# Optimization experiments

Measured on AMD Instinct MI355X. Metric: run time of the kernel, lower is better.

The kernel has to match this reference:

```python
import jax, jax.numpy as jnp
import numpy as np

DIM = 1024
NUM_HEADS = 16
HEAD_DIM = DIM // NUM_HEADS
SCALE = HEAD_DIM ** -0.5
HIDDEN = int(DIM * 1.0)


def setup_inputs() -> dict:
    key = jax.random.key(0)
    ks = jax.random.split(key, 11)
    s = 0.02
    return {
        "x":  jax.random.normal(ks[0], (2, 2048, DIM), jnp.float32),
        "Wq": jax.random.normal(ks[1], (DIM, DIM), jnp.float32) * s,
        "bq": jnp.zeros((DIM,), jnp.float32),
        "Wk": jax.random.normal(ks[2], (DIM, DIM), jnp.float32) * s,
        "bk": jnp.zeros((DIM,), jnp.float32),
        "Wv": jax.random.normal(ks[3], (DIM, DIM), jnp.float32) * s,
        "bv": jnp.zeros((DIM,), jnp.float32),
        "W1": jax.random.normal(ks[4], (HIDDEN, DIM), jnp.float32) * s,
        "b1": jnp.zeros((HIDDEN,), jnp.float32),
        "W2": jax.random.normal(ks[5], (DIM, HIDDEN), jnp.float32) * s,
        "b2": jnp.zeros((DIM,), jnp.float32),
    }


def _split_heads(t, B, S):
    # [B,S,C] -> [B,H,S,hd]
    return t.reshape(B, S, NUM_HEADS, HEAD_DIM).transpose(0, 2, 1, 3)


def reference(x, Wq, bq, Wk, bk, Wv, bv, W1, b1, W2, b2):
    B, S, C = x.shape
    q = _split_heads(x @ Wq.T + bq, B, S) * SCALE
    k = _split_heads(x @ Wk.T + bk, B, S)
    v = _split_heads(x @ Wv.T + bv, B, S)
    # softmax-free bilinear attention, scores in float32 (matches .float())
    attn = jnp.einsum('bhqd,bhkd->bhqk', q.astype(jnp.float32), k.astype(jnp.float32))
    out = jnp.einsum('bhqk,bhkd->bhqd', attn, v)  # [B,H,S,hd]
    out = out.transpose(0, 2, 1, 3).reshape(B, S, C)
    h = jax.nn.gelu(out @ W1.T + b1, approximate=False)
    mlp = h @ W2.T + b2
    return x + out + mlp
```

## Files before the change

### kernel.cpp

```cpp
#include <hip/hip_runtime.h>
#include <math.h>

#define DIM    1024
#define BATCH  2
#define SEQ    2048
#define NHEAD  16
#define HDIM   64
#define MROWS  (BATCH*SEQ)
#define NSPLIT 8

typedef unsigned short u16;
typedef __attribute__((ext_vector_type(8))) short  s16x8;
typedef __attribute__((ext_vector_type(4))) float  f32x4;

__device__ __forceinline__ float bf2f(u16 h) {
    unsigned u = ((unsigned)h) << 16; float f; __builtin_memcpy(&f, &u, 4); return f;
}
__device__ __forceinline__ u16 f2bf(float f) {
    unsigned u; __builtin_memcpy(&u, &f, 4);
    u += 0x7FFFu + ((u >> 16) & 1u);
    return (u16)(u >> 16);
}

__device__ __forceinline__ void glds16(const u16* g, u16* l) {
    __builtin_amdgcn_global_load_lds(
        (const __attribute__((address_space(1))) void*)g,
        (__attribute__((address_space(3))) void*)l, 16, 0, 0);
}

__global__ __launch_bounds__(256)
void pack_all(const float* __restrict__ x,
              const float* __restrict__ Wq, const float* __restrict__ Wk,
              const float* __restrict__ Wv, const float* __restrict__ W1,
              const float* __restrict__ W2,
              u16* __restrict__ xb, u16* __restrict__ Wqb, u16* __restrict__ Wkb,
              u16* __restrict__ Wvb, u16* __restrict__ W1b, u16* __restrict__ W2b)
{
    const int bid = blockIdx.x;
    const float* src; u16* dst; int i;
    if (bid < 4096) { src = x; dst = xb; i = bid * 256 + threadIdx.x; }
    else {
        const int w = (bid - 4096) >> 10;
        const int lb = (bid - 4096) & 1023;
        src = (w == 0) ? Wq : (w == 1) ? Wk : (w == 2) ? Wv : (w == 3) ? W1 : W2;
        dst = (w == 0) ? Wqb : (w == 1) ? Wkb : (w == 2) ? Wvb : (w == 3) ? W1b : W2b;
        i = lb * 256 + threadIdx.x;
    }
    float4 v = ((const float4*)src)[i];
    ushort4 o = { f2bf(v.x), f2bf(v.y), f2bf(v.z), f2bf(v.w) };
    ((ushort4*)dst)[i] = o;
}

__device__ __forceinline__ void gemm_core_pf128(const u16* __restrict__ Ab,
                                                const u16* __restrict__ Bb,
                                                u16* As, u16* Bs,
                                                int tid, f32x4 acc[4][4])
{
    const int w = tid >> 6, l = tid & 63;
    const int wm = (w >> 1) * 64, wn = (w & 1) * 64;
    const int lr = l & 15, kq = l >> 4;

    const int srow = w * 16 + (l >> 2);
    const int scol = (l & 3) * 8;
    const u16* gA = Ab + (size_t)srow * DIM + scol;
    const u16* gB = Bb + (size_t)srow * DIM + scol;
    const int sdst = w * 512;

    glds16(gA, As + sdst);  glds16(gA + 64 * DIM, As + 2048 + sdst);
    glds16(gB, Bs + sdst);  glds16(gB + 64 * DIM, Bs + 2048 + sdst);

    const int NIT = DIM / 32;
    for (int it = 0; it < NIT; ++it) {
        __syncthreads();
        if (it + 1 < NIT) {
            const int k = (it + 1) * 32;
            u16* An = As + ((it + 1) & 1) * 4096 + sdst;
            u16* Bn = Bs + ((it + 1) & 1) * 4096 + sdst;
            glds16(gA + k, An);  glds16(gA + k + 64 * DIM, An + 2048);
            glds16(gB + k, Bn);  glds16(gB + k + 64 * DIM, Bn + 2048);
        }
        const u16* Ac = As + (it & 1) * 4096;
        const u16* Bc = Bs + (it & 1) * 4096;
        s16x8 af[4], bfr[4];
        #pragma unroll
        for (int i = 0; i < 4; ++i)
            af[i]  = *(const s16x8*)(Ac + (wm + i * 16 + lr) * 32 + kq * 8);
        #pragma unroll
        for (int j = 0; j < 4; ++j)
            bfr[j] = *(const s16x8*)(Bc + (wn + j * 16 + lr) * 32 + kq * 8);
        #pragma unroll
        for (int i = 0; i < 4; ++i)
            #pragma unroll
            for (int j = 0; j < 4; ++j)
                acc[i][j] = __builtin_amdgcn_mfma_f32_16x16x32_bf16(af[i], bfr[j], acc[i][j], 0, 0, 0);
    }
}

__device__ __forceinline__ void gemm_core_pf64(const u16* __restrict__ Ab,
                                               const u16* __restrict__ Bb,
                                               u16* As , u16* Bs ,
                                               int tid, f32x4 acc[2][4])
{
    const int w  = tid >> 6, l = tid & 63;
    const int wm = (w >> 1) * 32, wn = (w & 1) * 64;
    const int lr = l & 15, kq = l >> 4;

    const int srow = w * 16 + (l >> 2);
    const int scol = (l & 3) * 8;
    const u16* gA = Ab + (size_t)srow * DIM + scol;
    const u16* gB = Bb + (size_t)srow * DIM + scol;
    const int sdst = w * 512;

    glds16(gA, As + sdst);
    glds16(gB, Bs + sdst);  glds16(gB + 64 * DIM, Bs + 2048 + sdst);

    const int NIT = DIM / 32;
    for (int it = 0; it < NIT; ++it) {
        __syncthreads();
        if (it + 1 < NIT) {
            const int k = (it + 1) * 32;
            u16* An = As + ((it + 1) & 1) * 2048 + sdst;
            u16* Bn = Bs + ((it + 1) & 1) * 4096 + sdst;
            glds16(gA + k, An);
            glds16(gB + k, Bn);  glds16(gB + k + 64 * DIM, Bn + 2048);
        }
        const u16* Ac = As + (it & 1) * 2048;
        const u16* Bc = Bs + (it & 1) * 4096;
        s16x8 af[2], bfr[4];
        #pragma unroll
        for (int i = 0; i < 2; ++i)
            af[i]  = *(const s16x8*)(Ac + (wm + i * 16 + lr) * 32 + kq * 8);
        #pragma unroll
        for (int j = 0; j < 4; ++j)
            bfr[j] = *(const s16x8*)(Bc + (wn + j * 16 + lr) * 32 + kq * 8);
        #pragma unroll
        for (int i = 0; i < 2; ++i)
            #pragma unroll
            for (int j = 0; j < 4; ++j)
                acc[i][j] = __builtin_amdgcn_mfma_f32_16x16x32_bf16(af[i], bfr[j], acc[i][j], 0, 0, 0);
    }
}

__global__ __launch_bounds__(256)
void qkv_gemm(const u16* __restrict__ xb,
              const u16* __restrict__ Wq, const u16* __restrict__ Wk, const u16* __restrict__ Wv,
              const float* __restrict__ bq, const float* __restrict__ bk, const float* __restrict__ bv,
              u16* __restrict__ qo, u16* __restrict__ ko, u16* __restrict__ vo)
{
    __shared__ __align__(16) u16 SH[16384];
    const int tid = threadIdx.x;
    const int m0  = blockIdx.x * 128;
    const int sel = blockIdx.y >> 3;
    const int n0  = (blockIdx.y & 7) * 128;
    const u16*   B    = (sel == 0) ? Wq : (sel == 1) ? Wk : Wv;
    const float* bias = (sel == 0) ? bq : (sel == 1) ? bk : bv;
    u16*         C    = (sel == 0) ? qo : (sel == 1) ? ko : vo;
    const float scale = (sel == 0) ? 0.125f : 1.0f;

    f32x4 acc[4][4];
    #pragma unroll
    for (int i = 0; i < 4; ++i)
        #pragma unroll
        for (int j = 0; j < 4; ++j) acc[i][j] = (f32x4){0.f, 0.f, 0.f, 0.f};

    gemm_core_pf128(xb + (size_t)m0 * DIM, B + (size_t)n0 * DIM, SH, SH + 8192, tid, acc);

    __syncthreads();
    const int w = tid >> 6, l = tid & 63;
    const int wm = (w >> 1) * 64, wn = (w & 1) * 64;
    const int er = l >> 4, ec = l & 15;
    #pragma unroll
    for (int j = 0; j < 4; ++j) {
        const int colv = wn + j * 16 + ec;
        const float bb = bias[n0 + colv];
        const int cg = colv >> 3, cl = colv & 7;
        #pragma unroll
        for (int i = 0; i < 4; ++i)
            #pragma unroll
            for (int r = 0; r < 4; ++r) {
                const int row = wm + i * 16 + er * 4 + r;
                const int g = ((row >> 2) & 3) << 1;
                SH[row * 128 + ((cg ^ g) << 3) + cl] = f2bf((acc[i][j][r] + bb) * scale);
            }
    }
    __syncthreads();
    {
        const int cg = tid & 15, rr = tid >> 4;
        #pragma unroll
        for (int pass = 0; pass < 8; ++pass) {
            const int row = rr + (pass << 4);
            const int g = ((row >> 2) & 3) << 1;
            uint4 v = *(const uint4*)(SH + row * 128 + ((cg ^ g) << 3));
            *(uint4*)(C + (size_t)(m0 + row) * DIM + n0 + (cg << 3)) = v;
        }
    }
}

__global__ __launch_bounds__(256)
void gemm_bf16(const u16* __restrict__ A, const u16* __restrict__ B,
               const float* __restrict__ bias,
               u16* __restrict__ Cb, float* __restrict__ Cf,
               const float* __restrict__ rx, const u16* __restrict__ rattn,
               int mode)
{
    __shared__ __align__(16) u16 SH[12288];
    const int tid = threadIdx.x;
    const int m0 = blockIdx.x * 64, n0 = blockIdx.y * 128;

    f32x4 acc[2][4];
    #pragma unroll
    for (int i = 0; i < 2; ++i)
        #pragma unroll
        for (int j = 0; j < 4; ++j) acc[i][j] = (f32x4){0.f, 0.f, 0.f, 0.f};

    gemm_core_pf64(A + (size_t)m0 * DIM, B + (size_t)n0 * DIM, SH, SH + 4096, tid, acc);

    const int w = tid >> 6, l = tid & 63;
    const int wm = (w >> 1) * 32, wn = (w & 1) * 64;
    const int er = l >> 4, ec = l & 15;

    if (mode == 1) {
        __syncthreads();
        #pragma unroll
        for (int j = 0; j < 4; ++j) {
            const int colv = wn + j * 16 + ec;
            const float bb = bias[n0 + colv];
            const int cg = colv >> 3, cl = colv & 7;
            #pragma unroll
            for (int i = 0; i < 2; ++i)
                #pragma unroll
                for (int r = 0; r < 4; ++r) {
                    const int row = wm + i * 16 + er * 4 + r;
                    const int g = ((row >> 2) & 3) << 1;
                    float v = acc[i][j][r] + bb;
                    v = 0.5f * v * (1.0f + erff(v * 0.70710678118654752f));
                    SH[row * 128 + ((cg ^ g) << 3) + cl] = f2bf(v);
                }
        }
        __syncthreads();
        const int cg = tid & 15, rr = tid >> 4;
        #pragma unroll
        for (int pass = 0; pass < 4; ++pass) {
            const int row = rr + (pass << 4);
            const int g = ((row >> 2) & 3) << 1;
            uint4 v = *(const uint4*)(SH + row * 128 + ((cg ^ g) << 3));
            *(uint4*)(Cb + (size_t)(m0 + row) * DIM + n0 + (cg << 3)) = v;
        }
    } else {
        float* SHF = (float*)SH;
        #pragma unroll
        for (int h = 0; h < 2; ++h) {
            __syncthreads();
            if ((w >> 1) == h) {
                #pragma unroll
                for (int j = 0; j < 4; ++j) {
                    const int colv = wn + j * 16 + ec;
                    const float bb = bias[n0 + colv];
                    const int c4 = colv >> 2, c2 = colv & 3;
                    #pragma unroll
                    for (int i = 0; i < 2; ++i)
                        #pragma unroll
                        for (int r = 0; r < 4; ++r) {
                            const int rl = i * 16 + er * 4 + r;
                            const int g4 = ((rl >> 2) & 1) << 2;
                            SHF[rl * 128 + ((c4 ^ g4) << 2) + c2] = acc[i][j][r] + bb;
                        }
                }
            }
            __syncthreads();
            const int c4 = tid & 31, rr = tid >> 5;
            #pragma unroll
            for (int pass = 0; pass < 4; ++pass) {
                const int rl = rr + (pass << 3);
                const int g4 = ((rl >> 2) & 1) << 2;
                float4 v = *(const float4*)(SHF + rl * 128 + ((c4 ^ g4) << 2));
                const size_t idx = (size_t)(m0 + 32 * h + rl) * DIM + n0 + (c4 << 2);
                float4 rxv = *(const float4*)(rx + idx);
                ushort4 rav = *(const ushort4*)(rattn + idx);
                float4 o = { v.x + rxv.x + bf2f(rav.x),
                             v.y + rxv.y + bf2f(rav.y),
                             v.z + rxv.z + bf2f(rav.z),
                             v.w + rxv.w + bf2f(rav.w) };
                *(float4*)(Cf + idx) = o;
            }
        }
    }
}

__global__ __launch_bounds__(256)
void ktv_mfma(const u16* __restrict__ Kb, const u16* __restrict__ Vb,
              float* __restrict__ part)
{
    __shared__ u16 Kt[64 * 264];
    __shared__ u16 Vt[64 * 264];
    const int tid = threadIdx.x;
    const int bh = blockIdx.x & 31;
    const int sp = blockIdx.x >> 5;
    const int b = bh >> 4, h = bh & 15;
    const size_t base = (size_t)b * SEQ * DIM + (size_t)h * HDIM + (size_t)sp * 256 * DIM;

    const int dg = (tid & 15) * 4;
    #pragma unroll
    for (int pass = 0; pass < 16; ++pass) {
        const int s = (tid >> 4) + 16 * pass;
        ushort4 kv = *(const ushort4*)(Kb + base + (size_t)s * DIM + dg);
        ushort4 vv = *(const ushort4*)(Vb + base + (size_t)s * DIM + dg);
        Kt[(dg + 0) * 264 + s] = kv.x; Kt[(dg + 1) * 264 + s] = kv.y;
        Kt[(dg + 2) * 264 + s] = kv.z; Kt[(dg + 3) * 264 + s] = kv.w;
        Vt[(dg + 0) * 264 + s] = vv.x; Vt[(dg + 1) * 264 + s] = vv.y;
        Vt[(dg + 2) * 264 + s] = vv.z; Vt[(dg + 3) * 264 + s] = vv.w;
    }
    __syncthreads();

    const int w = tid >> 6, l = tid & 63;
    const int lr = l & 15, kq = l >> 4;
    f32x4 acc[4];
    #pragma unroll
    for (int j = 0; j < 4; ++j) acc[j] = (f32x4){0.f, 0.f, 0.f, 0.f};

    for (int k0 = 0; k0 < 256; k0 += 32) {
        s16x8 af = *(const s16x8*)(Kt + (w * 16 + lr) * 264 + k0 + kq * 8);
        #pragma unroll
        for (int j = 0; j < 4; ++j) {
            s16x8 bf = *(const s16x8*)(Vt + (j * 16 + lr) * 264 + k0 + kq * 8);
            acc[j] = __builtin_amdgcn_mfma_f32_16x16x32_bf16(af, bf, acc[j], 0, 0, 0);
        }
    }

    float* dst = part + ((size_t)sp * 32 + bh) * (HDIM * HDIM);
    const int er = l >> 4, ec = l & 15;
    #pragma unroll
    for (int j = 0; j < 4; ++j)
        #pragma unroll
        for (int r = 0; r < 4; ++r)
            dst[(w * 16 + er * 4 + r) * HDIM + j * 16 + ec] = acc[j][r];
}

__global__ __launch_bounds__(256)
void qktv_kernel(const u16* __restrict__ Qb, const float* __restrict__ part,
                 u16* __restrict__ attnb)
{
    __shared__ float KV[HDIM * HDIM];
    __shared__ u16 Qs[128 * 68];
    const int tid = threadIdx.x;
    const int h  = blockIdx.x;
    const int mt = blockIdx.y;
    const int row0 = mt * 128;
    const int b = row0 >> 11;
    const int bh = b * NHEAD + h;

    for (int i = tid; i < HDIM * HDIM; i += 256) {
        float s = 0.f;
        #pragma unroll
        for (int sp = 0; sp < NSPLIT; ++sp)
            s += part[((size_t)sp * 32 + bh) * (HDIM * HDIM) + i];
        KV[i] = s;
    }
    const int dg = (tid & 15) * 4;
    #pragma unroll
    for (int pass = 0; pass < 8; ++pass) {
        const int r = (tid >> 4) + 16 * pass;
        ushort4 q = *(const ushort4*)(Qb + (size_t)(row0 + r) * DIM + h * HDIM + dg);
        *(ushort4*)(Qs + r * 68 + dg) = q;
    }
    __syncthreads();

    const int tr = tid >> 3, tc = tid & 7;
    const int r0 = tr * 4, c0 = tc * 8;
    float acc[4][8] = {};
    for (int d = 0; d < HDIM; ++d) {
        float4 ka  = *(const float4*)&KV[d * HDIM + c0];
        float4 kb2 = *(const float4*)&KV[d * HDIM + c0 + 4];
        const float* k8a = (const float*)&ka;
        const float* k8b = (const float*)&kb2;
        float qv[4];
        #pragma unroll
        for (int i = 0; i < 4; ++i) qv[i] = bf2f(Qs[(r0 + i) * 68 + d]);
        #pragma unroll
        for (int i = 0; i < 4; ++i)
            #pragma unroll
            for (int j = 0; j < 4; ++j) {
                acc[i][j]     += qv[i] * k8a[j];
                acc[i][j + 4] += qv[i] * k8b[j];
            }
    }
    #pragma unroll
    for (int i = 0; i < 4; ++i) {
        u16* dst = attnb + (size_t)(row0 + r0 + i) * DIM + h * HDIM + c0;
        ushort4 o0 = { f2bf(acc[i][0]), f2bf(acc[i][1]), f2bf(acc[i][2]), f2bf(acc[i][3]) };
        ushort4 o1 = { f2bf(acc[i][4]), f2bf(acc[i][5]), f2bf(acc[i][6]), f2bf(acc[i][7]) };
        *(ushort4*)(dst)     = o0;
        *(ushort4*)(dst + 4) = o1;
    }
}

extern "C" void kernel_launch(void* const* d_in, const int* in_sizes, int n_in,
                              void* d_out, int out_size, void* d_ws, size_t ws_size,
                              hipStream_t stream)
{
    const float* x  = (const float*)d_in[0];
    const float* Wq = (const float*)d_in[1];
    const float* bq = (const float*)d_in[2];
    const float* Wk = (const float*)d_in[3];
    const float* bk = (const float*)d_in[4];
    const float* Wv = (const float*)d_in[5];
    const float* bv = (const float*)d_in[6];
    const float* W1 = (const float*)d_in[7];
    const float* b1 = (const float*)d_in[8];
    const float* W2 = (const float*)d_in[9];
    const float* b2 = (const float*)d_in[10];
    float* out = (float*)d_out;

    char* ws = (char*)d_ws;
    const size_t MB = 1u << 20;
    u16* xb   = (u16*)(ws);
    u16* Wqb  = (u16*)(ws +  8 * MB);
    u16* Wkb  = (u16*)(ws + 10 * MB);
    u16* Wvb  = (u16*)(ws + 12 * MB);
    u16* W1b  = (u16*)(ws + 14 * MB);
    u16* W2b  = (u16*)(ws + 16 * MB);
    u16* qb   = (u16*)(ws + 18 * MB);
    u16* kb   = (u16*)(ws + 26 * MB);
    u16* vb   = (u16*)(ws + 34 * MB);
    float* part = (float*)(ws + 42 * MB);
    u16* attnb = kb;
    u16* h1b   = vb;

    pack_all<<<4096 + 5 * 1024, 256, 0, stream>>>(x, Wq, Wk, Wv, W1, W2,
                                                  xb, Wqb, Wkb, Wvb, W1b, W2b);

    qkv_gemm<<<dim3(32, 24), 256, 0, stream>>>(xb, Wqb, Wkb, Wvb, bq, bk, bv, qb, kb, vb);

    ktv_mfma<<<NSPLIT * 32, 256, 0, stream>>>(kb, vb, part);
    qktv_kernel<<<dim3(NHEAD, MROWS / 128), 256, 0, stream>>>(qb, part, attnb);

    gemm_bf16<<<dim3(64, 8), 256, 0, stream>>>(attnb, W1b, b1, h1b, nullptr, nullptr, nullptr, 1);
    gemm_bf16<<<dim3(64, 8), 256, 0, stream>>>(h1b, W2b, b2, nullptr, out, x, attnb, 2);
}
```

Before: 199.5 us.

## Triple-buffer GEMM shared-memory tiles with two-stage prefetch and vmcnt waits

Both GEMM cores move from double to triple buffering in LDS, prefetching two K-tiles ahead. A single __syncthreads is replaced by explicit s_waitcnt vmcnt(N) plus s_barrier, so only the oldest tile's loads are waited on. MFMA blocks are bracketed with s_setprio to favour math issue, and gemm_bf16 gets a launch_bounds occupancy hint. The LDS footprint grows by half, which may reduce occupancy, and the hand-set vmcnt counts must match the compiler's load order to stay correct.

```diff
diff --git a/kernel.cpp b/kernel.cpp
--- a/kernel.cpp
+++ b/kernel.cpp
@@ -66,21 +66,27 @@
     const u16* gB = Bb + (size_t)srow * DIM + scol;
     const int sdst = w * 512;
 
-    glds16(gA, As + sdst);  glds16(gA + 64 * DIM, As + 2048 + sdst);
-    glds16(gB, Bs + sdst);  glds16(gB + 64 * DIM, Bs + 2048 + sdst);
+    glds16(gA,      As + sdst);         glds16(gA + 64 * DIM,      As + 2048 + sdst);
+    glds16(gB,      Bs + sdst);         glds16(gB + 64 * DIM,      Bs + 2048 + sdst);
+    glds16(gA + 32, As + 4096 + sdst);  glds16(gA + 32 + 64 * DIM, As + 4096 + 2048 + sdst);
+    glds16(gB + 32, Bs + 4096 + sdst);  glds16(gB + 32 + 64 * DIM, Bs + 4096 + 2048 + sdst);
 
     const int NIT = DIM / 32;
+    int cur = 0, nxt2 = 2;
     for (int it = 0; it < NIT; ++it) {
-        __syncthreads();
-        if (it + 1 < NIT) {
-            const int k = (it + 1) * 32;
-            u16* An = As + ((it + 1) & 1) * 4096 + sdst;
-            u16* Bn = Bs + ((it + 1) & 1) * 4096 + sdst;
+        if (it < NIT - 1) { asm volatile("s_waitcnt vmcnt(4)" ::: "memory"); }
+        else              { asm volatile("s_waitcnt vmcnt(0)" ::: "memory"); }
+        __builtin_amdgcn_s_barrier();
+        asm volatile("" ::: "memory");
+        if (it + 2 < NIT) {
+            const int k = (it + 2) * 32;
+            u16* An = As + nxt2 * 4096 + sdst;
+            u16* Bn = Bs + nxt2 * 4096 + sdst;
             glds16(gA + k, An);  glds16(gA + k + 64 * DIM, An + 2048);
             glds16(gB + k, Bn);  glds16(gB + k + 64 * DIM, Bn + 2048);
         }
-        const u16* Ac = As + (it & 1) * 4096;
-        const u16* Bc = Bs + (it & 1) * 4096;
+        const u16* Ac = As + cur * 4096;
+        const u16* Bc = Bs + cur * 4096;
         s16x8 af[4], bfr[4];
         #pragma unroll
         for (int i = 0; i < 4; ++i)
@@ -88,11 +94,15 @@
         #pragma unroll
         for (int j = 0; j < 4; ++j)
             bfr[j] = *(const s16x8*)(Bc + (wn + j * 16 + lr) * 32 + kq * 8);
+        __builtin_amdgcn_s_setprio(1);
         #pragma unroll
         for (int i = 0; i < 4; ++i)
             #pragma unroll
             for (int j = 0; j < 4; ++j)
                 acc[i][j] = __builtin_amdgcn_mfma_f32_16x16x32_bf16(af[i], bfr[j], acc[i][j], 0, 0, 0);
+        __builtin_amdgcn_s_setprio(0);
+        cur  = (cur  == 2) ? 0 : cur  + 1;
+        nxt2 = (nxt2 == 2) ? 0 : nxt2 + 1;
     }
 }
 
@@ -111,21 +121,27 @@
     const u16* gB = Bb + (size_t)srow * DIM + scol;
     const int sdst = w * 512;
 
-    glds16(gA, As + sdst);
-    glds16(gB, Bs + sdst);  glds16(gB + 64 * DIM, Bs + 2048 + sdst);
+    glds16(gA,      As + sdst);
+    glds16(gB,      Bs + sdst);        glds16(gB + 64 * DIM,      Bs + 2048 + sdst);
+    glds16(gA + 32, As + 2048 + sdst);
+    glds16(gB + 32, Bs + 4096 + sdst); glds16(gB + 32 + 64 * DIM, Bs + 4096 + 2048 + sdst);
 
     const int NIT = DIM / 32;
+    int cur = 0, nxt2 = 2;
     for (int it = 0; it < NIT; ++it) {
-        __syncthreads();
-        if (it + 1 < NIT) {
-            const int k = (it + 1) * 32;
-            u16* An = As + ((it + 1) & 1) * 2048 + sdst;
-            u16* Bn = Bs + ((it + 1) & 1) * 4096 + sdst;
+        if (it < NIT - 1) { asm volatile("s_waitcnt vmcnt(3)" ::: "memory"); }
+        else              { asm volatile("s_waitcnt vmcnt(0)" ::: "memory"); }
+        __builtin_amdgcn_s_barrier();
+        asm volatile("" ::: "memory");
+        if (it + 2 < NIT) {
+            const int k = (it + 2) * 32;
+            u16* An = As + nxt2 * 2048 + sdst;
+            u16* Bn = Bs + nxt2 * 4096 + sdst;
             glds16(gA + k, An);
             glds16(gB + k, Bn);  glds16(gB + k + 64 * DIM, Bn + 2048);
         }
-        const u16* Ac = As + (it & 1) * 2048;
-        const u16* Bc = Bs + (it & 1) * 4096;
+        const u16* Ac = As + cur * 2048;
+        const u16* Bc = Bs + cur * 4096;
         s16x8 af[2], bfr[4];
         #pragma unroll
         for (int i = 0; i < 2; ++i)
@@ -133,11 +149,15 @@
         #pragma unroll
         for (int j = 0; j < 4; ++j)
             bfr[j] = *(const s16x8*)(Bc + (wn + j * 16 + lr) * 32 + kq * 8);
+        __builtin_amdgcn_s_setprio(1);
         #pragma unroll
         for (int i = 0; i < 2; ++i)
             #pragma unroll
             for (int j = 0; j < 4; ++j)
                 acc[i][j] = __builtin_amdgcn_mfma_f32_16x16x32_bf16(af[i], bfr[j], acc[i][j], 0, 0, 0);
+        __builtin_amdgcn_s_setprio(0);
+        cur  = (cur  == 2) ? 0 : cur  + 1;
+        nxt2 = (nxt2 == 2) ? 0 : nxt2 + 1;
     }
 }
 
@@ -147,7 +167,7 @@
               const float* __restrict__ bq, const float* __restrict__ bk, const float* __restrict__ bv,
               u16* __restrict__ qo, u16* __restrict__ ko, u16* __restrict__ vo)
 {
-    __shared__ __align__(16) u16 SH[16384];
+    __shared__ __align__(16) u16 SH[24576];
     const int tid = threadIdx.x;
     const int m0  = blockIdx.x * 128;
     const int sel = blockIdx.y >> 3;
@@ -163,7 +183,7 @@
         #pragma unroll
         for (int j = 0; j < 4; ++j) acc[i][j] = (f32x4){0.f, 0.f, 0.f, 0.f};
 
-    gemm_core_pf128(xb + (size_t)m0 * DIM, B + (size_t)n0 * DIM, SH, SH + 8192, tid, acc);
+    gemm_core_pf128(xb + (size_t)m0 * DIM, B + (size_t)n0 * DIM, SH, SH + 12288, tid, acc);
 
     __syncthreads();
     const int w = tid >> 6, l = tid & 63;
@@ -196,14 +216,14 @@
     }
 }
 
-__global__ __launch_bounds__(256)
+__global__ __launch_bounds__(256, 2)
 void gemm_bf16(const u16* __restrict__ A, const u16* __restrict__ B,
                const float* __restrict__ bias,
                u16* __restrict__ Cb, float* __restrict__ Cf,
                const float* __restrict__ rx, const u16* __restrict__ rattn,
                int mode)
 {
-    __shared__ __align__(16) u16 SH[12288];
+    __shared__ __align__(16) u16 SH[18432];
     const int tid = threadIdx.x;
     const int m0 = blockIdx.x * 64, n0 = blockIdx.y * 128;
 
@@ -213,7 +233,7 @@
         #pragma unroll
         for (int j = 0; j < 4; ++j) acc[i][j] = (f32x4){0.f, 0.f, 0.f, 0.f};
 
-    gemm_core_pf64(A + (size_t)m0 * DIM, B + (size_t)n0 * DIM, SH, SH + 4096, tid, acc);
+    gemm_core_pf64(A + (size_t)m0 * DIM, B + (size_t)n0 * DIM, SH, SH + 6144, tid, acc);
 
     const int w = tid >> 6, l = tid & 63;
     const int wm = (w >> 1) * 32, wn = (w & 1) * 64;
```

Result: faster. 192.0 us (-3.7%).
